# Performance work log

Hardware: AMD Instinct MI355X
Metric: run time of the kernel (lower is better)

Reference implementation:

```python
import jax, jax.numpy as jnp
import numpy as np
from functools import partial

B, T_OUT, T_IN, L, D_IN, D_ATT = 8, 256, 512, 128, 128, 128


def setup_inputs() -> dict:
    key = jax.random.key(0)
    ks = jax.random.split(key, 8)
    s = 0.05  # small init scale for numerical stability
    return {
        "inputs": jax.random.normal(ks[0], (B, T_OUT, D_IN), jnp.float32),
        "attended_inputs": jax.random.normal(ks[1], (B, T_IN, D_ATT), jnp.float32),
        "lstm_kernel": jax.random.normal(ks[2], (D_IN, 4 * L), jnp.float32) * s,
        "lstm_rec_kernel": jax.random.normal(ks[3], (L, 4 * L), jnp.float32) * s,
        "lstm_bias": jnp.zeros((4 * L,), jnp.float32),
        "W1": jax.random.normal(ks[4], (D_ATT, L), jnp.float32) * s,
        "b1": jnp.zeros((L,), jnp.float32),
        "W2": jax.random.normal(ks[5], (L, L), jnp.float32) * s,
        "b2": jnp.zeros((L,), jnp.float32),
        "W3": jax.random.normal(ks[6], (L, 1), jnp.float32) * s,
        "b3": jnp.zeros((1,), jnp.float32),
    }


def _lstm(x, Wk, Wr, b):
    # x: (B, T, D_in). Keras gate order: i, f, c(g), o. Zero initial state.
    Bq = x.shape[0]
    h0 = jnp.zeros((Bq, L), x.dtype)
    c0 = jnp.zeros((Bq, L), x.dtype)
    xz = jnp.einsum('btd,dk->btk', x, Wk) + b  # precompute input projection

    def step(carry, zt):
        h, c = carry
        z = zt + h @ Wr
        i, f, g, o = jnp.split(z, 4, axis=-1)
        c_new = jax.nn.sigmoid(f) * c + jax.nn.sigmoid(i) * jnp.tanh(g)
        h_new = jax.nn.sigmoid(o) * jnp.tanh(c_new)
        return (h_new, c_new), h_new

    (h_T, c_T), hs = jax.lax.scan(step, (h0, c0), jnp.swapaxes(xz, 0, 1))
    return jnp.swapaxes(hs, 0, 1), h_T, c_T  # (B, T, L), (B, L), (B, L)


def reference(inputs, attended_inputs, lstm_kernel, lstm_rec_kernel, lstm_bias,
              W1, b1, W2, b2, W3, b3):
    # setup_attended: keys = dense1(attended_inputs)
    keys = attended_inputs @ W1 + b1  # (B, T_in, L)
    x, h, c = _lstm(inputs, lstm_kernel, lstm_rec_kernel, lstm_bias)  # (B, T_out, L)
    q = x @ W2 + b2  # (B, T_out, L)
    # Bahdanau additive score: tanh(keys[:,None] + q[:,:,None]) . W3 -> (B, T_out, T_in)
    t = jnp.tanh(keys[:, None, :, :] + q[:, :, None, :])  # (B, T_out, T_in, L)
    scores = jnp.einsum('bqkl,l->bqk', t, W3[:, 0]) + b3[0]
    attn = jax.nn.softmax(scores, axis=-1)
    weighted = jnp.einsum('bqk,bkd->bqd', attn, attended_inputs)  # (B, T_out, D_att)
    out = jnp.concatenate([x, weighted], axis=2)  # (B, T_out, L + D_att)
    return out, h, c
```

## Files before the change

kernel.cpp:

```cpp
#include <hip/hip_runtime.h>
#include <hip/hip_bf16.h>

#define XF_OFF   0
#define PROG_OFF 524288
#define XZ_OFF   1048576
#define KEYS_OFF 2097152
#define OUT_H    524288
#define OUT_C    525312

#define LDS_BARRIER() __asm__ __volatile__("s_waitcnt lgkmcnt(0)\n\ts_barrier" ::: "memory")

typedef _Float16 f16x8 __attribute__((ext_vector_type(8)));
typedef float fx4 __attribute__((ext_vector_type(4)));

__device__ __forceinline__ float fast_rcp(float x) { return __builtin_amdgcn_rcpf(x); }
__device__ __forceinline__ float fast_sig(float v) { return fast_rcp(1.f + __expf(-v)); }
__device__ __forceinline__ float fast_tanh(float v) { return 2.f * fast_rcp(1.f + __expf(-2.f * v)) - 1.f; }

__global__ __launch_bounds__(256)
void prologue_k(const float* __restrict__ inp, const float* __restrict__ Wk,
                const float* __restrict__ bias, const float* __restrict__ att,
                const float* __restrict__ W1, const float* __restrict__ b1,
                float* __restrict__ ws) {
  __shared__ float ar[8][128];
  __shared__ float ar2[16][128];
  const int tid = threadIdx.x;

  if (blockIdx.x < 256) {
    _Float16* xz16 = (_Float16*)(ws + XZ_OFF);
    const int row0 = blockIdx.x * 8;
    for (int i = tid; i < 8 * 128; i += 256) ar[i >> 7][i & 127] = inp[row0 * 128 + i];
    __syncthreads();
    float acc[8][2];
    const float bb0 = bias[tid], bb1 = bias[tid + 256];
#pragma unroll
    for (int r = 0; r < 8; ++r) { acc[r][0] = bb0; acc[r][1] = bb1; }
    for (int d = 0; d < 128; d += 4) {
      float w0a = Wk[(d + 0) * 512 + tid], w0b = Wk[(d + 0) * 512 + tid + 256];
      float w1a = Wk[(d + 1) * 512 + tid], w1b = Wk[(d + 1) * 512 + tid + 256];
      float w2a = Wk[(d + 2) * 512 + tid], w2b = Wk[(d + 2) * 512 + tid + 256];
      float w3a = Wk[(d + 3) * 512 + tid], w3b = Wk[(d + 3) * 512 + tid + 256];
#pragma unroll
      for (int r = 0; r < 8; ++r) {
        float4 a4 = *(const float4*)&ar[r][d];
        acc[r][0] += a4.x * w0a + a4.y * w1a + a4.z * w2a + a4.w * w3a;
        acc[r][1] += a4.x * w0b + a4.y * w1b + a4.z * w2b + a4.w * w3b;
      }
    }
    const int u = tid & 127, g0 = tid >> 7;
#pragma unroll
    for (int r = 0; r < 8; ++r) {
      const int row = row0 + r, b = row >> 8, t = row & 255;
      const int base = ((t * 8 + b) * 128 + u) * 4;
      xz16[base + g0]     = (_Float16)acc[r][0];
      xz16[base + g0 + 2] = (_Float16)acc[r][1];
    }
    return;
  }

  if (blockIdx.x == 256 && tid < 2) ((int*)(ws + PROG_OFF))[tid] = 0;
  const int kb = blockIdx.x - 256;
  const int row0 = kb * 16;
  const int bq = row0 >> 9, k0 = row0 & 511;
  for (int i = tid; i < 16 * 128; i += 256) ar2[i >> 7][i & 127] = att[row0 * 128 + i];
  __syncthreads();
  const int l = tid & 127, r0 = tid >> 7;
  float acc[8];
  const float bl = b1[l];
#pragma unroll
  for (int i = 0; i < 8; ++i) acc[i] = bl;
  for (int d = 0; d < 128; d += 4) {
    float w0 = W1[(d + 0) * 128 + l], w1 = W1[(d + 1) * 128 + l];
    float w2 = W1[(d + 2) * 128 + l], w3 = W1[(d + 3) * 128 + l];
#pragma unroll
    for (int i = 0; i < 8; ++i) {
      float4 a4 = *(const float4*)&ar2[r0 * 8 + i][d];
      acc[i] += a4.x * w0 + a4.y * w1 + a4.z * w2 + a4.w * w3;
    }
  }
  float* kT = ws + KEYS_OFF + (bq * 128 + l) * 512 + k0 + r0 * 8;
  float4 lo = {acc[0], acc[1], acc[2], acc[3]};
  float4 hi = {acc[4], acc[5], acc[6], acc[7]};
  *(float4*)kT = lo;
  *(float4*)(kT + 4) = hi;
}

struct ScanS { _Float16 hb[2][576]; };
struct AttnS {
  float xr[4][128];
  float qp[4][128];
  float sc[4][512];
  float kc[8][516];
  float w3s[128];
};

__global__ __launch_bounds__(512)
void fused_scan_attn(const float* __restrict__ Wrf, const float* __restrict__ att,
                     const float* __restrict__ W2c, const float* __restrict__ b2c,
                     const float* __restrict__ W3c, const float* __restrict__ b3c,
                     float* __restrict__ ws, float* __restrict__ out) {
  __shared__ __align__(16) char smem[29312];
  const int tid = threadIdx.x;
  int* prog = (int*)(ws + PROG_OFF);
  float* xf = ws + XF_OFF;

  if (blockIdx.x >= 2) {
    AttnS* A = (AttnS*)smem;
    const int wkr = blockIdx.x - 2;
    if (tid < 128) A->w3s[tid] = W3c[tid];
    const int l = tid & 127, r0 = tid >> 7;
    for (int ci = 0; ci < 2; ++ci) {
      const int c = 2 * wkr + ci;
      const int b = c >> 6, q0 = (c & 63) * 4;
      if (tid == 0) {
        while (__hip_atomic_load(&prog[b >> 2], __ATOMIC_RELAXED, __HIP_MEMORY_SCOPE_AGENT) < q0 + 4)
          __builtin_amdgcn_s_sleep(16);
      }
      __syncthreads();
      const int row = b * 256 + q0 + r0;
      const float xv = __hip_atomic_load(&xf[row * 128 + l], __ATOMIC_RELAXED, __HIP_MEMORY_SCOPE_AGENT);
      A->xr[r0][l] = xv;
      out[row * 256 + l] = xv;
      __syncthreads();
      float qa = b2c[l];
      for (int d = 0; d < 128; d += 4) {
        float4 x4 = *(const float4*)&A->xr[r0][d];
        qa += x4.x * W2c[(d + 0) * 128 + l] + x4.y * W2c[(d + 1) * 128 + l]
            + x4.z * W2c[(d + 2) * 128 + l] + x4.w * W2c[(d + 3) * 128 + l];
      }
      A->qp[r0][l] = qa;
      const float b3v = b3c[0];
      float acc0 = b3v, acc1 = b3v, acc2 = b3v, acc3 = b3v;
      const float* keysT = ws + KEYS_OFF + b * (128 * 512);
      for (int cc = 0; cc < 128; cc += 8) {
        __syncthreads();
        for (int i = tid; i < 8 * 512; i += 512)
          A->kc[i >> 9][i & 511] = keysT[(cc + (i >> 9)) * 512 + (i & 511)];
        __syncthreads();
        for (int lp = 0; lp < 8; ++lp) {
          const float qv = A->qp[r0][cc + lp];
          const float wv = A->w3s[cc + lp];
          acc0 += fast_tanh(A->kc[lp][l]       + qv) * wv;
          acc1 += fast_tanh(A->kc[lp][l + 128] + qv) * wv;
          acc2 += fast_tanh(A->kc[lp][l + 256] + qv) * wv;
          acc3 += fast_tanh(A->kc[lp][l + 384] + qv) * wv;
        }
      }
      A->sc[r0][l]       = acc0;
      A->sc[r0][l + 128] = acc1;
      A->sc[r0][l + 256] = acc2;
      A->sc[r0][l + 384] = acc3;
      __syncthreads();
      {
        const int wave = tid >> 6, lane = tid & 63;
        if (wave < 4) {
          float v[8];
#pragma unroll
          for (int i = 0; i < 8; ++i) v[i] = A->sc[wave][lane + i * 64];
          float m = v[0];
#pragma unroll
          for (int i = 1; i < 8; ++i) m = fmaxf(m, v[i]);
#pragma unroll
          for (int off = 32; off > 0; off >>= 1) m = fmaxf(m, __shfl_xor(m, off));
          float e[8], s = 0.f;
#pragma unroll
          for (int i = 0; i < 8; ++i) { e[i] = __expf(v[i] - m); s += e[i]; }
#pragma unroll
          for (int off = 32; off > 0; off >>= 1) s += __shfl_xor(s, off);
          const float inv = fast_rcp(s);
#pragma unroll
          for (int i = 0; i < 8; ++i) A->sc[wave][lane + i * 64] = e[i] * inv;
        }
      }
      __syncthreads();
      const float* attb = att + b * (512 * 128);
      float wa = 0.f;
      for (int k = 0; k < 512; k += 4) {
        float4 p4 = *(const float4*)&A->sc[r0][k];
        wa += p4.x * attb[(k + 0) * 128 + l] + p4.y * attb[(k + 1) * 128 + l]
            + p4.z * attb[(k + 2) * 128 + l] + p4.w * attb[(k + 3) * 128 + l];
      }
      out[row * 256 + 128 + l] = wa;
    }
    return;
  }

  ScanS* S = (ScanS*)smem;
  const _Float16* xz16 = (const _Float16*)(ws + XZ_OFF);
  const int b_base = blockIdx.x * 4;
  const int w = tid >> 6, lane = tid & 63;
  const int q = lane >> 4, p = lane & 15;
  const int b = p & 3, isel = p >> 2;
  const int u = 16 * w + 4 * isel + q;
  const int bg = b_base + b;

  f16x8 afr[4][4];
#pragma unroll
  for (int i = 0; i < 4; ++i) {
    const int col = (p & 3) * 128 + 16 * w + 4 * i + (p >> 2);
#pragma unroll
    for (int kt = 0; kt < 4; ++kt)
#pragma unroll
      for (int j = 0; j < 8; ++j)
        afr[i][kt][j] = (_Float16)Wrf[(kt * 32 + q * 8 + j) * 512 + col];
  }
  {
    _Float16* hp = &S->hb[0][0];
    for (int i = tid; i < 2 * 576; i += 512) hp[i] = (_Float16)0.f;
  }
  const fx4 zeroC = {0.f, 0.f, 0.f, 0.f};
  float cst = 0.f, hval = 0.f;
  const _Float16* xp = xz16 + (bg * 128 + u) * 4;
  uint2 pf0 = *(const uint2*)(xp);
  uint2 pf1 = *(const uint2*)(xp + 4096);
  uint2 pf2 = *(const uint2*)(xp + 8192);
  __syncthreads();

  const int brow = b * 144;
  for (int t = 0; t < 256; ++t) {
    const _Float16* hrow = &S->hb[t & 1][brow];
    f16x8 bfr[4];
#pragma unroll
    for (int kt = 0; kt < 4; ++kt)
      bfr[kt] = *(const f16x8*)&hrow[kt * 32 + q * 8];
    fx4 acc[4];
#pragma unroll
    for (int i = 0; i < 4; ++i)
      acc[i] = __builtin_amdgcn_mfma_f32_16x16x32_f16(afr[i][0], bfr[0], zeroC, 0, 0, 0);
#pragma unroll
    for (int kt = 1; kt < 4; ++kt)
#pragma unroll
      for (int i = 0; i < 4; ++i)
        acc[i] = __builtin_amdgcn_mfma_f32_16x16x32_f16(afr[i][kt], bfr[kt], acc[i], 0, 0, 0);

    float z[4];
#pragma unroll
    for (int r = 0; r < 4; ++r) {
      float s01 = (isel & 1) ? acc[1][r] : acc[0][r];
      float s23 = (isel & 1) ? acc[3][r] : acc[2][r];
      z[r] = (isel & 2) ? s23 : s01;
    }

    uint2 cur = pf0;
    pf0 = pf1; pf1 = pf2;

    const _Float16* cf = (const _Float16*)&cur;
    const float zi = z[0] + (float)cf[0];
    const float zf = z[1] + (float)cf[1];
    const float zg = z[2] + (float)cf[2];
    const float zo = z[3] + (float)cf[3];
    cst = fast_sig(zf) * cst + fast_sig(zi) * fast_tanh(zg);
    hval = fast_sig(zo) * fast_tanh(cst);
    S->hb[(t + 1) & 1][brow + u] = (_Float16)hval;
    __hip_atomic_store(&xf[(bg * 256 + t) * 128 + u], hval,
                       __ATOMIC_RELAXED, __HIP_MEMORY_SCOPE_AGENT);

    if ((t & 15) == 15) {
      __syncthreads();
      if (tid == 0)
        __hip_atomic_store(&prog[blockIdx.x], t + 1,
                           __ATOMIC_RELAXED, __HIP_MEMORY_SCOPE_AGENT);
    } else {
      LDS_BARRIER();
    }
    const int t3 = (t + 3 < 256) ? t + 3 : 255;
    pf2 = *(const uint2*)(xp + t3 * 4096);
  }
  out[OUT_H + bg * 128 + u] = hval;
  out[OUT_C + bg * 128 + u] = cst;
}

extern "C" void kernel_launch(void* const* d_in, const int* in_sizes, int n_in,
                              void* d_out, int out_size, void* d_ws, size_t ws_size,
                              hipStream_t stream) {
  const float* inputs   = (const float*)d_in[0];
  const float* attended = (const float*)d_in[1];
  const float* Wk       = (const float*)d_in[2];
  const float* Wr       = (const float*)d_in[3];
  const float* bias     = (const float*)d_in[4];
  const float* W1       = (const float*)d_in[5];
  const float* b1       = (const float*)d_in[6];
  const float* W2       = (const float*)d_in[7];
  const float* b2       = (const float*)d_in[8];
  const float* W3       = (const float*)d_in[9];
  const float* b3       = (const float*)d_in[10];
  float* out = (float*)d_out;
  float* ws = (float*)d_ws;

  hipLaunchKernelGGL(prologue_k, dim3(512), dim3(256), 0, stream,
                     inputs, Wk, bias, attended, W1, b1, ws);
  hipLaunchKernelGGL(fused_scan_attn, dim3(258), dim3(512), 0, stream,
                     Wr, attended, W2, b2, W3, b3, ws, out);
}
```

Measured before the change: 345.1 us.

## Fold tanh into sigmoid form, reorder attention chunk assignment, prioritize scan waves

Rewrites the additive score as sum(2*w3*sigmoid(2x)) - sum(w3) by pre-scaling keys and queries by -2*log2(e). Each tanh then costs one exp2 and one reciprocal, with fewer multiplies. Attention blocks now pair an early chunk with a late one so work is balanced against scan progress. Scan blocks get higher wave priority, and they publish progress every 32 steps instead of 16. The grid grows by two blocks that exit at once, which keeps the attention blocks' indexing consistent. The coarser progress updates may delay attention consumers, and the sigmoid form slightly changes rounding.

```diff
diff --git a/kernel.cpp b/kernel.cpp
--- a/kernel.cpp
+++ b/kernel.cpp
@@ -10,12 +10,20 @@
 
 #define LDS_BARRIER() __asm__ __volatile__("s_waitcnt lgkmcnt(0)\n\ts_barrier" ::: "memory")
 
+#if __has_builtin(__builtin_amdgcn_exp2f)
+#define EXP2F __builtin_amdgcn_exp2f
+#else
+#define EXP2F exp2f
+#endif
+
 typedef _Float16 f16x8 __attribute__((ext_vector_type(8)));
 typedef float fx4 __attribute__((ext_vector_type(4)));
 
 __device__ __forceinline__ float fast_rcp(float x) { return __builtin_amdgcn_rcpf(x); }
 __device__ __forceinline__ float fast_sig(float v) { return fast_rcp(1.f + __expf(-v)); }
 __device__ __forceinline__ float fast_tanh(float v) { return 2.f * fast_rcp(1.f + __expf(-2.f * v)) - 1.f; }
+
+#define CSCALE (-2.8853900817779268f)
 
 __global__ __launch_bounds__(256)
 void prologue_k(const float* __restrict__ inp, const float* __restrict__ Wk,
@@ -104,13 +112,22 @@
   int* prog = (int*)(ws + PROG_OFF);
   float* xf = ws + XF_OFF;
 
+  if (blockIdx.x == 256 || blockIdx.x == 257) return;
+
   if (blockIdx.x >= 2) {
     AttnS* A = (AttnS*)smem;
-    const int wkr = blockIdx.x - 2;
-    if (tid < 128) A->w3s[tid] = W3c[tid];
+    const int wkr = (blockIdx.x < 256) ? (int)blockIdx.x - 2 : (int)blockIdx.x - 4;
+    int cA = wkr, cB = 511 - wkr;
+    if ((cA & 63) > (cB & 63)) { int tmp = cA; cA = cB; cB = tmp; }
+    if (tid < 128) A->w3s[tid] = 2.f * W3c[tid];
+    float sw3 = 0.f;
+    for (int ll = 0; ll < 128; ll += 4) {
+      float4 w4 = *(const float4*)&W3c[ll];
+      sw3 += w4.x + w4.y + w4.z + w4.w;
+    }
     const int l = tid & 127, r0 = tid >> 7;
     for (int ci = 0; ci < 2; ++ci) {
-      const int c = 2 * wkr + ci;
+      const int c = ci ? cB : cA;
       const int b = c >> 6, q0 = (c & 63) * 4;
       if (tid == 0) {
         while (__hip_atomic_load(&prog[b >> 2], __ATOMIC_RELAXED, __HIP_MEMORY_SCOPE_AGENT) < q0 + 4)
@@ -128,22 +145,22 @@
         qa += x4.x * W2c[(d + 0) * 128 + l] + x4.y * W2c[(d + 1) * 128 + l]
             + x4.z * W2c[(d + 2) * 128 + l] + x4.w * W2c[(d + 3) * 128 + l];
       }
-      A->qp[r0][l] = qa;
-      const float b3v = b3c[0];
-      float acc0 = b3v, acc1 = b3v, acc2 = b3v, acc3 = b3v;
+      A->qp[r0][l] = CSCALE * qa;
+      const float base = b3c[0] - sw3;
+      float acc0 = base, acc1 = base, acc2 = base, acc3 = base;
       const float* keysT = ws + KEYS_OFF + b * (128 * 512);
       for (int cc = 0; cc < 128; cc += 8) {
         __syncthreads();
         for (int i = tid; i < 8 * 512; i += 512)
-          A->kc[i >> 9][i & 511] = keysT[(cc + (i >> 9)) * 512 + (i & 511)];
+          A->kc[i >> 9][i & 511] = CSCALE * keysT[(cc + (i >> 9)) * 512 + (i & 511)];
         __syncthreads();
         for (int lp = 0; lp < 8; ++lp) {
           const float qv = A->qp[r0][cc + lp];
           const float wv = A->w3s[cc + lp];
-          acc0 += fast_tanh(A->kc[lp][l]       + qv) * wv;
-          acc1 += fast_tanh(A->kc[lp][l + 128] + qv) * wv;
-          acc2 += fast_tanh(A->kc[lp][l + 256] + qv) * wv;
-          acc3 += fast_tanh(A->kc[lp][l + 384] + qv) * wv;
+          acc0 += fast_rcp(1.f + EXP2F(A->kc[lp][l]       + qv)) * wv;
+          acc1 += fast_rcp(1.f + EXP2F(A->kc[lp][l + 128] + qv)) * wv;
+          acc2 += fast_rcp(1.f + EXP2F(A->kc[lp][l + 256] + qv)) * wv;
+          acc3 += fast_rcp(1.f + EXP2F(A->kc[lp][l + 384] + qv)) * wv;
         }
       }
       A->sc[r0][l]       = acc0;
@@ -185,6 +202,7 @@
     return;
   }
 
+  __builtin_amdgcn_s_setprio(1);
   ScanS* S = (ScanS*)smem;
   const _Float16* xz16 = (const _Float16*)(ws + XZ_OFF);
   const int b_base = blockIdx.x * 4;
@@ -255,7 +273,7 @@
     __hip_atomic_store(&xf[(bg * 256 + t) * 128 + u], hval,
                        __ATOMIC_RELAXED, __HIP_MEMORY_SCOPE_AGENT);
 
-    if ((t & 15) == 15) {
+    if ((t & 31) == 31) {
       __syncthreads();
       if (tid == 0)
         __hip_atomic_store(&prog[blockIdx.x], t + 1,
@@ -289,6 +307,6 @@
 
   hipLaunchKernelGGL(prologue_k, dim3(512), dim3(256), 0, stream,
                      inputs, Wk, bias, attended, W1, b1, ws);
-  hipLaunchKernelGGL(fused_scan_attn, dim3(258), dim3(512), 0, stream,
+  hipLaunchKernelGGL(fused_scan_attn, dim3(260), dim3(512), 0, stream,
                      Wr, attended, W2, b2, W3, b3, ws, out);
 }
```

After: 329.6 us. 1.05x faster.
